# Kernel tuning notes

Hardware: AMD Instinct MI355X
Metric: run time of the kernel (lower is better)

The kernel has to match this reference:

```python
import jax, jax.numpy as jnp
import numpy as np
from functools import partial

K = 3
P = K * K * K          # 27 kernel points
G = 2                  # groups
PAD = 1
STRIDE = 1
DIL = 1
AXIS_SCALE = (0.5, 1.0, 1.0)   # (x, y, z) offset axis scale
CUR_SCALE = 0.5                # warmup scale at global_step=0
EPS = 1e-5


def setup_inputs() -> dict:
    key = jax.random.key(0)
    ks = jax.random.split(key, 8)
    C, OC = 64, 64
    N, D, H, W = 1, 32, 32, 32
    inp = {
        "x": jax.random.normal(ks[0], (N, C, D, H, W), jnp.float32),
        "dw_w": jax.random.normal(ks[1], (C, 1, K, K, K), jnp.float32) * 0.1,
        "gn_w": jnp.ones((C,), jnp.float32),
        "gn_b": jnp.zeros((C,), jnp.float32),
        "inp_w": jax.random.normal(ks[2], (C, C), jnp.float32) * (1.0 / np.sqrt(C)),
        "inp_b": jnp.zeros((C,), jnp.float32),
        # offset/mask weights are zero-init in the module; use small random values
        # so the deformable sampling path is exercised nontrivially.
        "off_w": jax.random.normal(ks[3], (C, G * P * 3), jnp.float32) * 0.01,
        "off_b": jnp.zeros((G * P * 3,), jnp.float32),
        "mask_w": jax.random.normal(ks[4], (C, G * P), jnp.float32) * 0.01,
        "mask_b": jnp.tile(jnp.full((P,), -5.0, jnp.float32).at[P // 2].set(0.0), (G,)),
        "out_w": jax.random.normal(ks[5], (C, OC), jnp.float32) * (1.0 / np.sqrt(C)),
        "out_b": jnp.zeros((OC,), jnp.float32),
    }
    return inp


def _trilinear(vol, loc):
    # vol: [Dp, Hp, Wp, gc]; loc: [..., 3] with (x, y, z) in [-1, 1]
    # grid_sample semantics: align_corners=False, padding_mode='zeros'
    Dp, Hp, Wp, _ = vol.shape
    ix = (loc[..., 0] + 1.0) * 0.5 * Wp - 0.5
    iy = (loc[..., 1] + 1.0) * 0.5 * Hp - 0.5
    iz = (loc[..., 2] + 1.0) * 0.5 * Dp - 0.5
    x0f, y0f, z0f = jnp.floor(ix), jnp.floor(iy), jnp.floor(iz)
    fx, fy, fz = ix - x0f, iy - y0f, iz - z0f
    x0, y0, z0 = x0f.astype(jnp.int32), y0f.astype(jnp.int32), z0f.astype(jnp.int32)
    out = jnp.zeros(loc.shape[:-1] + (vol.shape[-1],), vol.dtype)
    for dz in (0, 1):
        wz = fz if dz else 1.0 - fz
        cz = z0 + dz
        for dy in (0, 1):
            wy = fy if dy else 1.0 - fy
            cy = y0 + dy
            for dx in (0, 1):
                wx = fx if dx else 1.0 - fx
                cx = x0 + dx
                valid = ((cz >= 0) & (cz < Dp) & (cy >= 0) & (cy < Hp)
                         & (cx >= 0) & (cx < Wp))
                v = vol[jnp.clip(cz, 0, Dp - 1),
                        jnp.clip(cy, 0, Hp - 1),
                        jnp.clip(cx, 0, Wp - 1)]  # [..., gc]
                out = out + (wz * wy * wx * valid.astype(vol.dtype))[..., None] * v
    return out


def _forward(x, dw_w, gn_w, gn_b, inp_w, inp_b, off_w, off_b,
             mask_w, mask_b, out_w, out_b):
    N, C, D, H, W = x.shape
    gc = C // G
    # --- dw_conv: depthwise conv3d + GroupNorm(1, C) + GELU ---
    xc = jax.lax.conv_general_dilated(
        x, dw_w, window_strides=(1, 1, 1), padding=[(PAD, PAD)] * 3,
        dimension_numbers=("NCDHW", "OIDHW", "NCDHW"), feature_group_count=C)
    mu = xc.mean(axis=(1, 2, 3, 4), keepdims=True)
    var = ((xc - mu) ** 2).mean(axis=(1, 2, 3, 4), keepdims=True)
    xn = (xc - mu) * jax.lax.rsqrt(var + EPS)
    xn = xn * gn_w[None, :, None, None, None] + gn_b[None, :, None, None, None]
    x1 = jnp.transpose(jax.nn.gelu(xn), (0, 2, 3, 4, 1))       # [N,D,H,W,C]
    # --- offset / mask / input projection ---
    offset = x1 @ off_w + off_b                                  # [N,D,H,W,G*P*3]
    mask = jax.nn.softmax(
        (x1 @ mask_w + mask_b).reshape(N, D, H, W, G, P), axis=-1)
    xp = jnp.transpose(x, (0, 2, 3, 4, 1)) @ inp_w + inp_b       # [N,D,H,W,C]
    # --- core deformable sampling ---
    x_pad = jnp.pad(xp, ((0, 0), (PAD, PAD), (PAD, PAD), (PAD, PAD), (0, 0)))
    Dp, Hp, Wp = D + 2 * PAD, H + 2 * PAD, W + 2 * PAD
    Do = (D + 2 * PAD - DIL * (K - 1) - 1) // STRIDE + 1
    Ho = (H + 2 * PAD - DIL * (K - 1) - 1) // STRIDE + 1
    Wo = (W + 2 * PAD - DIL * (K - 1) - 1) // STRIDE + 1
    # reference grid (x/Wp, y/Hp, z/Dp)
    zc, yc, xc_ = jnp.meshgrid(jnp.arange(Do, dtype=jnp.float32),
                               jnp.arange(Ho, dtype=jnp.float32),
                               jnp.arange(Wo, dtype=jnp.float32), indexing="ij")
    ref = jnp.stack(((xc_ * STRIDE + PAD + 0.5) / Wp,
                     (yc * STRIDE + PAD + 0.5) / Hp,
                     (zc * STRIDE + PAD + 0.5) / Dp), axis=-1)   # [Do,Ho,Wo,3]
    # kernel grid
    lin = jnp.linspace(-(K - 1) // 2, (K - 1) // 2, K, dtype=jnp.float32)
    kz, ky, kx = jnp.meshgrid(lin, lin, lin, indexing="ij")
    kgrid = jnp.stack((kx * DIL / Wp, ky * DIL / Hp, kz * DIL / Dp),
                      axis=-1).reshape(P, 3)
    off = offset.reshape(N, Do, Ho, Wo, G, P, 3)
    off_norm = off / jnp.array([Wp, Hp, Dp], jnp.float32)
    axis = jnp.array(AXIS_SCALE, jnp.float32)
    loc = (ref[None, :, :, :, None, None, :]
           + kgrid[None, None, None, None, None, :, :]
           + off_norm * axis * CUR_SCALE)
    loc = loc * 2.0 - 1.0                                        # [N,Do,Ho,Wo,G,P,3]
    vol = jnp.transpose(x_pad.reshape(N, Dp, Hp, Wp, G, gc),
                        (0, 4, 1, 2, 3, 5))                      # [N,G,Dp,Hp,Wp,gc]
    locs = jnp.transpose(loc, (0, 4, 1, 2, 3, 5, 6))             # [N,G,Do,Ho,Wo,P,3]
    sampled = jax.vmap(jax.vmap(_trilinear))(vol, locs)          # [N,G,Do,Ho,Wo,P,gc]
    out = jnp.einsum("ngdhwpc,ndhwgp->ndhwgc", sampled, mask)
    out = out.reshape(N, Do, Ho, Wo, C)
    return out @ out_w + out_b                                   # [N,Do,Ho,Wo,OC]


def reference(x, dw_w, gn_w, gn_b, inp_w, inp_b, off_w, off_b,
              mask_w, mask_b, out_w, out_b):
    return _forward(x, dw_w, gn_w, gn_b, inp_w, inp_b, off_w, off_b,
                    mask_w, mask_b, out_w, out_b)
```

## Files before the change

### kernel.cpp

```cpp
#include <hip/hip_runtime.h>
#include <hip/hip_fp16.h>
#include <math.h>

#define SP 32768
#define PW 38
#define PW2 (PW*PW)
#define PVOX (PW*PW*PW)
#define OMS 228

typedef short bf16x8 __attribute__((ext_vector_type(8)));
typedef unsigned short u16x4 __attribute__((ext_vector_type(4)));
typedef float f32x4 __attribute__((ext_vector_type(4)));

__device__ __forceinline__ unsigned short f2b(float f) {
    unsigned u = __float_as_uint(f);
    u = (u + 0x7FFFu + ((u >> 16) & 1u)) >> 16;
    return (unsigned short)u;
}
__device__ __forceinline__ float b2f1(unsigned short s) {
    return __uint_as_float(((unsigned)s) << 16);
}
__device__ __forceinline__ __half2 h2(unsigned u) {
    return *reinterpret_cast<__half2*>(&u);
}

__global__ void k_front(const float* __restrict__ x, const float* __restrict__ dw,
                        const float* __restrict__ off_w, const float* __restrict__ mask_w,
                        const float* __restrict__ off_b, const float* __restrict__ mask_b,
                        const float* __restrict__ inp_w, const float* __restrict__ out_w,
                        unsigned short* __restrict__ WcatB, float* __restrict__ bcat,
                        unsigned short* __restrict__ inpB, unsigned short* __restrict__ outB,
                        unsigned short* __restrict__ x_tb,
                        unsigned short* __restrict__ xcb, float* __restrict__ partials) {
    int bb = blockIdx.x, tid = threadIdx.x;
    if (bb < 88) {
        int idx = bb * 256 + tid;
        int j = idx >> 6, k = idx & 63;
        if (j < 224) {
            float v = 0.f;
            if (j < 162) v = off_w[k * 162 + j];
            else if (j < 216) v = mask_w[k * 54 + (j - 162)];
            WcatB[j * 64 + k] = f2b(v);
            if (k == 0) bcat[j] = (j < 162) ? off_b[j] : (j < 216 ? mask_b[j - 162] : 0.f);
        } else if (j < 288) {
            outB[(j - 224) * 64 + k] = f2b(out_w[k * 64 + (j - 224)]);
        } else {
            inpB[(j - 288) * 64 + k] = f2b(inp_w[k * 64 + (j - 288)]);
        }
        return;
    }
    if (bb < 600) {
        __shared__ unsigned short tile[64][66];
        int s0 = (bb - 88) * 64;
        int row = tid >> 6, lane = tid & 63;
        for (int c = row; c < 64; c += 4)
            tile[c][lane] = f2b(x[(size_t)c * SP + s0 + lane]);
        __syncthreads();
        for (int r = row; r < 64; r += 4)
            x_tb[(size_t)(s0 + r) * 64 + lane] = tile[lane][r];
        return;
    }
    int b3 = bb - 600;
    int e = b3 * 256 + tid;
    int c = e >> 15, s = e & 32767;
    int d = s >> 10, h = (s >> 5) & 31, w = s & 31;
    const float* xs = x + (size_t)c * SP;
    const float* wt = dw + c * 27;
    float a = 0.f;
#pragma unroll
    for (int kd = 0; kd < 3; ++kd) {
        int zz = d + kd - 1; if ((unsigned)zz >= 32u) continue;
#pragma unroll
        for (int kh = 0; kh < 3; ++kh) {
            int yy = h + kh - 1; if ((unsigned)yy >= 32u) continue;
#pragma unroll
            for (int kw = 0; kw < 3; ++kw) {
                int xx = w + kw - 1; if ((unsigned)xx >= 32u) continue;
                a += xs[(zz << 10) + (yy << 5) + xx] * wt[kd * 9 + kh * 3 + kw];
            }
        }
    }
    xcb[e] = f2b(a);
    __shared__ float rs[256], rq[256];
    rs[tid] = a; rq[tid] = a * a;
    __syncthreads();
    for (int off = 128; off > 0; off >>= 1) {
        if (tid < off) { rs[tid] += rs[tid + off]; rq[tid] += rq[tid + off]; }
        __syncthreads();
    }
    if (tid == 0) {
        partials[b3 * 2 + 0] = rs[0];
        partials[b3 * 2 + 1] = rq[0];
    }
}

__global__ void k_mid(const unsigned short* __restrict__ xcb, const float* __restrict__ partials,
                      const float* __restrict__ gn_w, const float* __restrict__ gn_b,
                      unsigned short* __restrict__ x1b,
                      const unsigned short* __restrict__ x_tb,
                      const unsigned short* __restrict__ inpB,
                      const float* __restrict__ inp_b,
                      unsigned short* __restrict__ xpad) {
    int bb = blockIdx.x, tid = threadIdx.x;
    if (bb < 512) {
        __shared__ float rs[256], rq[256];
        __shared__ unsigned short tile[64][66];
        float a = 0.f, b = 0.f;
        for (int i = tid; i < 8192; i += 256) { a += partials[2 * i]; b += partials[2 * i + 1]; }
        rs[tid] = a; rq[tid] = b;
        __syncthreads();
        for (int off = 128; off > 0; off >>= 1) {
            if (tid < off) { rs[tid] += rs[tid + off]; rq[tid] += rq[tid + off]; }
            __syncthreads();
        }
        const float Minv = 1.f / 2097152.f;
        float mu = rs[0] * Minv;
        float var = rq[0] * Minv - mu * mu;
        float rsq = rsqrtf(var + 1e-5f);
        int s0 = bb * 64;
        int row = tid >> 6, lane = tid & 63;
        for (int c = row; c < 64; c += 4) {
            float v = (b2f1(xcb[(size_t)c * SP + s0 + lane]) - mu) * rsq * gn_w[c] + gn_b[c];
            float t2 = 1.5957691216057308f * (v + 0.044715f * v * v * v);
            tile[c][lane] = f2b(v / (1.f + __expf(-t2)));
        }
        __syncthreads();
        for (int r = row; r < 64; r += 4)
            x1b[(size_t)(s0 + r) * 64 + lane] = tile[lane][r];
        return;
    }
    if (bb < 1024) {
        int wv = tid >> 6, lane = tid & 63;
        int quad = lane >> 4, col = lane & 15;
        int s0 = (bb - 512) * 64 + wv * 16;
        bf16x8 a0 = *(const bf16x8*)(x_tb + (size_t)(s0 + col) * 64 + quad * 8);
        bf16x8 a1 = *(const bf16x8*)(x_tb + (size_t)(s0 + col) * 64 + 32 + quad * 8);
        int vp[4];
#pragma unroll
        for (int r = 0; r < 4; ++r) {
            int s = s0 + (quad << 2) + r;
            vp[r] = (((s >> 10) + 2) * PW + ((s >> 5) & 31) + 2) * PW + (s & 31) + 2;
        }
#pragma unroll
        for (int nt = 0; nt < 4; ++nt) {
            int n0 = nt * 16;
            bf16x8 b0 = *(const bf16x8*)(inpB + (n0 + col) * 64 + quad * 8);
            bf16x8 b1 = *(const bf16x8*)(inpB + (n0 + col) * 64 + 32 + quad * 8);
            f32x4 c = {0.f, 0.f, 0.f, 0.f};
            c = __builtin_amdgcn_mfma_f32_16x16x32_bf16(a0, b0, c, 0, 0, 0);
            c = __builtin_amdgcn_mfma_f32_16x16x32_bf16(a1, b1, c, 0, 0, 0);
            float bq = inp_b[n0 + col];
#pragma unroll
            for (int r = 0; r < 4; ++r)
                xpad[(size_t)vp[r] * 64 + n0 + col] =
                    __half_as_ushort(__float2half(c[r] + bq));
        }
        return;
    }
    int cblk = bb - 1024;
    int j = tid >> 4, c4 = tid & 15;
    u16x4 z = {0, 0, 0, 0};
#pragma unroll
    for (int k = 0; k < 4; ++k) {
        int v = cblk * 64 + k * 16 + j;
        if (v >= PVOX) break;
        int zz = v / PW2, r = v - zz * PW2, yy = r / PW, xx = r - yy * PW;
        if (zz < 2 || zz > 33 || yy < 2 || yy > 33 || xx < 2 || xx > 33)
            *(u16x4*)(xpad + (size_t)v * 64 + c4 * 4) = z;
    }
}

template<int P0, int NP>
__device__ __forceinline__ void sampleN(const float* __restrict__ orow,
                                        const float* __restrict__ mrow,
                                        const char* __restrict__ volc,
                                        float xb, float yb, float zb,
                                        float* __restrict__ acc) {
#pragma unroll
    for (int i = 0; i < NP; ++i) {
        const int p = P0 + i;
        const int px = p % 3, py = (p / 3) % 3, pz = p / 9;
        float ox = orow[p * 3 + 0], oy = orow[p * 3 + 1], oz = orow[p * 3 + 2];
        float mk = mrow[p];
        float ix = __builtin_fmaf(0.25f, ox, xb + (float)px);
        float iy = __builtin_fmaf(0.5f, oy, yb + (float)py);
        float iz = __builtin_fmaf(0.5f, oz, zb + (float)pz);
        ix = fminf(fmaxf(ix, 0.f), 36.f);
        iy = fminf(fmaxf(iy, 0.f), 36.f);
        iz = fminf(fmaxf(iz, 0.f), 36.f);
        float xf = floorf(ix), yf = floorf(iy), zf = floorf(iz);
        float fx = ix - xf, fy = iy - yf, fz = iz - zf;
        float fi = __builtin_fmaf(zf, (float)PW2, __builtin_fmaf(yf, (float)PW, xf));
        int ib = ((int)fi) << 7;
        const char* base = volc + ib;
        uint4 r000 = *(const uint4*)(base);
        uint4 r001 = *(const uint4*)(base + 128);
        uint4 r010 = *(const uint4*)(base + PW * 128);
        uint4 r011 = *(const uint4*)(base + PW * 128 + 128);
        uint4 r100 = *(const uint4*)(base + PW2 * 128);
        uint4 r101 = *(const uint4*)(base + PW2 * 128 + 128);
        uint4 r110 = *(const uint4*)(base + (PW2 + PW) * 128);
        uint4 r111 = *(const uint4*)(base + (PW2 + PW) * 128 + 128);
        __half2 fx2 = __float2half2_rn(fx);
        __half2 fy2 = __float2half2_rn(fy);
        __half2 fz2 = __float2half2_rn(fz);
        #define TRI(comp, ci)                                                   \
        {                                                                       \
            __half2 t0 = __hfma2(fx2, __hsub2(h2(r001.comp), h2(r000.comp)), h2(r000.comp)); \
            __half2 t1 = __hfma2(fx2, __hsub2(h2(r011.comp), h2(r010.comp)), h2(r010.comp)); \
            __half2 t2 = __hfma2(fx2, __hsub2(h2(r101.comp), h2(r100.comp)), h2(r100.comp)); \
            __half2 t3 = __hfma2(fx2, __hsub2(h2(r111.comp), h2(r110.comp)), h2(r110.comp)); \
            __half2 u0 = __hfma2(fy2, __hsub2(t1, t0), t0);                     \
            __half2 u1 = __hfma2(fy2, __hsub2(t3, t2), t2);                     \
            __half2 rr = __hfma2(fz2, __hsub2(u1, u0), u0);                     \
            float2 ff = __half22float2(rr);                                     \
            acc[2 * ci + 0] = __builtin_fmaf(mk, ff.x, acc[2 * ci + 0]);        \
            acc[2 * ci + 1] = __builtin_fmaf(mk, ff.y, acc[2 * ci + 1]);        \
        }
        TRI(x, 0) TRI(y, 1) TRI(z, 2) TRI(w, 3)
        #undef TRI
    }
}

__global__ void __launch_bounds__(128, 4) k_main(const unsigned short* __restrict__ x1b,
                                                 const unsigned short* __restrict__ xpad,
                                                 const unsigned short* __restrict__ WcatB,
                                                 const float* __restrict__ bcat,
                                                 const unsigned short* __restrict__ outB,
                                                 const float* __restrict__ out_b,
                                                 float* __restrict__ out) {
    __shared__ float om_s[16 * OMS];
    __shared__ unsigned short smb[16 * 72];
    int tid = threadIdx.x, wv = tid >> 6, lane = tid & 63;
    int quad = lane >> 4, col = lane & 15;
    int sb = ((blockIdx.x & 7) << 8) | (blockIdx.x >> 3);
    int s0 = sb * 16;
    {
        bf16x8 a0 = *(const bf16x8*)(x1b + (size_t)(s0 + col) * 64 + quad * 8);
        bf16x8 a1 = *(const bf16x8*)(x1b + (size_t)(s0 + col) * 64 + 32 + quad * 8);
        for (int jt = wv; jt < 14; jt += 2) {
            int n0 = jt * 16;
            bf16x8 b0 = *(const bf16x8*)(WcatB + (n0 + col) * 64 + quad * 8);
            bf16x8 b1 = *(const bf16x8*)(WcatB + (n0 + col) * 64 + 32 + quad * 8);
            f32x4 c = {0.f, 0.f, 0.f, 0.f};
            c = __builtin_amdgcn_mfma_f32_16x16x32_bf16(a0, b0, c, 0, 0, 0);
            c = __builtin_amdgcn_mfma_f32_16x16x32_bf16(a1, b1, c, 0, 0, 0);
            float bb = bcat[n0 + col];
            int n = n0 + col, slot;
            if (n < 162) slot = n + ((n >= 81) ? 3 : 0);
            else { int n2 = n - 162; slot = 168 + n2 + ((n2 >= 27) ? 1 : 0); }
            if (n < 216) {
#pragma unroll
                for (int r = 0; r < 4; ++r)
                    om_s[(quad * 4 + r) * OMS + slot] = c[r] + bb;
            }
        }
    }
    __syncthreads();
    {
        int row = lane >> 2, sub = lane & 3;
        int vloc = wv * 8 + (row >> 1), g = row & 1;
        float* m = &om_s[vloc * OMS + 168 + g * 28];
        float mv[7];
        float mx = -1e30f;
#pragma unroll
        for (int i = 0; i < 7; ++i) {
            int p = sub * 7 + i;
            mv[i] = (p < 27) ? m[p] : -1e30f;
            mx = fmaxf(mx, mv[i]);
        }
        mx = fmaxf(mx, __shfl_xor(mx, 1));
        mx = fmaxf(mx, __shfl_xor(mx, 2));
        float e[7], sm = 0.f;
#pragma unroll
        for (int i = 0; i < 7; ++i) { e[i] = __expf(mv[i] - mx); sm += e[i]; }
        sm += __shfl_xor(sm, 1);
        sm += __shfl_xor(sm, 2);
        float inv = 1.f / sm;
#pragma unroll
        for (int i = 0; i < 7; ++i) {
            int p = sub * 7 + i;
            if (p < 27) m[p] = e[i] * inv;
        }
    }
    {
        int v = wv * 8 + (lane >> 3);
        int oct = lane & 7, gg = oct >> 2;
        int sv = s0 + v;
        float zb = (float)((sv >> 10) + 1);
        float yb = (float)(((sv >> 5) & 31) + 1);
        float xb = (float)((sv & 31) + 1);
        const float* orow = &om_s[v * OMS + gg * 84];
        const float* mrow = &om_s[v * OMS + 168 + gg * 28];
        const char* volc = (const char*)xpad + oct * 16;
        float acc[8] = {0.f, 0.f, 0.f, 0.f, 0.f, 0.f, 0.f, 0.f};
        sampleN<0, 27>(orow, mrow, volc, xb, yb, zb, acc);
        bf16x8 sb8;
#pragma unroll
        for (int k = 0; k < 8; ++k) sb8[k] = (short)f2b(acc[k]);
        *(bf16x8*)(smb + v * 72 + oct * 8) = sb8;
    }
    __syncthreads();
    {
        bf16x8 oa0 = *(const bf16x8*)(smb + col * 72 + quad * 8);
        bf16x8 oa1 = *(const bf16x8*)(smb + col * 72 + 32 + quad * 8);
#pragma unroll
        for (int t = 0; t < 2; ++t) {
            int n0 = (wv + t * 2) * 16;
            bf16x8 b0 = *(const bf16x8*)(outB + (n0 + col) * 64 + quad * 8);
            bf16x8 b1 = *(const bf16x8*)(outB + (n0 + col) * 64 + 32 + quad * 8);
            f32x4 c = {0.f, 0.f, 0.f, 0.f};
            c = __builtin_amdgcn_mfma_f32_16x16x32_bf16(oa0, b0, c, 0, 0, 0);
            c = __builtin_amdgcn_mfma_f32_16x16x32_bf16(oa1, b1, c, 0, 0, 0);
            float bb = out_b[n0 + col];
#pragma unroll
            for (int r = 0; r < 4; ++r)
                out[(size_t)(s0 + quad * 4 + r) * 64 + n0 + col] = c[r] + bb;
        }
    }
}

extern "C" void kernel_launch(void* const* d_in, const int* in_sizes, int n_in,
                              void* d_out, int out_size, void* d_ws, size_t ws_size,
                              hipStream_t stream) {
    const float* x      = (const float*)d_in[0];
    const float* dw_w   = (const float*)d_in[1];
    const float* gn_w   = (const float*)d_in[2];
    const float* gn_b   = (const float*)d_in[3];
    const float* inp_w  = (const float*)d_in[4];
    const float* inp_b  = (const float*)d_in[5];
    const float* off_w  = (const float*)d_in[6];
    const float* off_b  = (const float*)d_in[7];
    const float* mask_w = (const float*)d_in[8];
    const float* mask_b = (const float*)d_in[9];
    const float* out_w  = (const float*)d_in[10];
    const float* out_b  = (const float*)d_in[11];

    char* B = (char*)d_ws;
    float*          partials = (float*)(B + 256);
    unsigned short* xcb      = (unsigned short*)(B + 65792);
    unsigned short* x1b      = (unsigned short*)(B + 8454400);
    unsigned short* x_tb     = (unsigned short*)(B + 12648704);
    unsigned short* xpad     = (unsigned short*)(B + 16843008);
    unsigned short* WcatB    = (unsigned short*)(B + 30890240);
    float*          bcat     = (float*)(B + 30918912);
    unsigned short* inpB     = (unsigned short*)(B + 30919936);
    unsigned short* outB     = (unsigned short*)(B + 30928128);
    float* out = (float*)d_out;

    k_front<<<8792, 256, 0, stream>>>(x, dw_w, off_w, mask_w, off_b, mask_b,
                                      inp_w, out_w, WcatB, bcat, inpB, outB,
                                      x_tb, xcb, partials);
    k_mid<<<512 + 512 + 858, 256, 0, stream>>>(xcb, partials, gn_w, gn_b, x1b,
                                               x_tb, inpB, inp_b, xpad);
    k_main<<<2048, 128, 0, stream>>>(x1b, xpad, WcatB, bcat, outB, out_b, out);
}
```

Baseline: 174.0 us.

## Double threads per block so each sampler lane handles four channels

The main kernel goes from 128 to 256 threads per block. Each deformable-sampling lane now covers 4 fp16 channels with 8-byte corner loads instead of 8 channels with 16-byte loads, which halves per-thread register and arithmetic work and doubles the number of threads in flight to hide gather latency. The softmax, offset GEMM and output GEMM work splits are re-mapped to 4 waves. In exchange, the offset/mask coordinate math is repeated twice as many times and each corner fetch is narrower.

```diff
diff --git a/kernel.cpp b/kernel.cpp
--- a/kernel.cpp
+++ b/kernel.cpp
@@ -170,15 +170,13 @@
     }
 }
 
-template<int P0, int NP>
-__device__ __forceinline__ void sampleN(const float* __restrict__ orow,
-                                        const float* __restrict__ mrow,
-                                        const char* __restrict__ volc,
-                                        float xb, float yb, float zb,
-                                        float* __restrict__ acc) {
-#pragma unroll
-    for (int i = 0; i < NP; ++i) {
-        const int p = P0 + i;
+__device__ __forceinline__ void sample27_4(const float* __restrict__ orow,
+                                           const float* __restrict__ mrow,
+                                           const char* __restrict__ volc,
+                                           float xb, float yb, float zb,
+                                           float* __restrict__ acc) {
+#pragma unroll
+    for (int p = 0; p < 27; ++p) {
         const int px = p % 3, py = (p / 3) % 3, pz = p / 9;
         float ox = orow[p * 3 + 0], oy = orow[p * 3 + 1], oz = orow[p * 3 + 2];
         float mk = mrow[p];
@@ -193,14 +191,14 @@
         float fi = __builtin_fmaf(zf, (float)PW2, __builtin_fmaf(yf, (float)PW, xf));
         int ib = ((int)fi) << 7;
         const char* base = volc + ib;
-        uint4 r000 = *(const uint4*)(base);
-        uint4 r001 = *(const uint4*)(base + 128);
-        uint4 r010 = *(const uint4*)(base + PW * 128);
-        uint4 r011 = *(const uint4*)(base + PW * 128 + 128);
-        uint4 r100 = *(const uint4*)(base + PW2 * 128);
-        uint4 r101 = *(const uint4*)(base + PW2 * 128 + 128);
-        uint4 r110 = *(const uint4*)(base + (PW2 + PW) * 128);
-        uint4 r111 = *(const uint4*)(base + (PW2 + PW) * 128 + 128);
+        uint2 r000 = *(const uint2*)(base);
+        uint2 r001 = *(const uint2*)(base + 128);
+        uint2 r010 = *(const uint2*)(base + PW * 128);
+        uint2 r011 = *(const uint2*)(base + PW * 128 + 128);
+        uint2 r100 = *(const uint2*)(base + PW2 * 128);
+        uint2 r101 = *(const uint2*)(base + PW2 * 128 + 128);
+        uint2 r110 = *(const uint2*)(base + (PW2 + PW) * 128);
+        uint2 r111 = *(const uint2*)(base + (PW2 + PW) * 128 + 128);
         __half2 fx2 = __float2half2_rn(fx);
         __half2 fy2 = __float2half2_rn(fy);
         __half2 fz2 = __float2half2_rn(fz);
@@ -217,12 +215,12 @@
             acc[2 * ci + 0] = __builtin_fmaf(mk, ff.x, acc[2 * ci + 0]);        \
             acc[2 * ci + 1] = __builtin_fmaf(mk, ff.y, acc[2 * ci + 1]);        \
         }
-        TRI(x, 0) TRI(y, 1) TRI(z, 2) TRI(w, 3)
+        TRI(x, 0) TRI(y, 1)
         #undef TRI
     }
 }
 
-__global__ void __launch_bounds__(128, 4) k_main(const unsigned short* __restrict__ x1b,
+__global__ void __launch_bounds__(256, 8) k_main(const unsigned short* __restrict__ x1b,
                                                  const unsigned short* __restrict__ xpad,
                                                  const unsigned short* __restrict__ WcatB,
                                                  const float* __restrict__ bcat,
@@ -238,7 +236,7 @@
     {
         bf16x8 a0 = *(const bf16x8*)(x1b + (size_t)(s0 + col) * 64 + quad * 8);
         bf16x8 a1 = *(const bf16x8*)(x1b + (size_t)(s0 + col) * 64 + 32 + quad * 8);
-        for (int jt = wv; jt < 14; jt += 2) {
+        for (int jt = wv; jt < 14; jt += 4) {
             int n0 = jt * 16;
             bf16x8 b0 = *(const bf16x8*)(WcatB + (n0 + col) * 64 + quad * 8);
             bf16x8 b1 = *(const bf16x8*)(WcatB + (n0 + col) * 64 + 32 + quad * 8);
@@ -258,65 +256,64 @@
     }
     __syncthreads();
     {
-        int row = lane >> 2, sub = lane & 3;
-        int vloc = wv * 8 + (row >> 1), g = row & 1;
+        int row = lane >> 3, sub = lane & 7;
+        int vloc = wv * 4 + (row >> 1), g = row & 1;
         float* m = &om_s[vloc * OMS + 168 + g * 28];
-        float mv[7];
+        float mv[4];
         float mx = -1e30f;
 #pragma unroll
-        for (int i = 0; i < 7; ++i) {
-            int p = sub * 7 + i;
+        for (int i = 0; i < 4; ++i) {
+            int p = sub * 4 + i;
             mv[i] = (p < 27) ? m[p] : -1e30f;
             mx = fmaxf(mx, mv[i]);
         }
         mx = fmaxf(mx, __shfl_xor(mx, 1));
         mx = fmaxf(mx, __shfl_xor(mx, 2));
-        float e[7], sm = 0.f;
-#pragma unroll
-        for (int i = 0; i < 7; ++i) { e[i] = __expf(mv[i] - mx); sm += e[i]; }
+        mx = fmaxf(mx, __shfl_xor(mx, 4));
+        float e[4], sm = 0.f;
+#pragma unroll
+        for (int i = 0; i < 4; ++i) { e[i] = __expf(mv[i] - mx); sm += e[i]; }
         sm += __shfl_xor(sm, 1);
         sm += __shfl_xor(sm, 2);
+        sm += __shfl_xor(sm, 4);
         float inv = 1.f / sm;
 #pragma unroll
-        for (int i = 0; i < 7; ++i) {
-            int p = sub * 7 + i;
+        for (int i = 0; i < 4; ++i) {
+            int p = sub * 4 + i;
             if (p < 27) m[p] = e[i] * inv;
         }
     }
     {
-        int v = wv * 8 + (lane >> 3);
-        int oct = lane & 7, gg = oct >> 2;
+        int v = wv * 4 + (lane >> 4);
+        int oc = lane & 15, gg = oc >> 3;
         int sv = s0 + v;
         float zb = (float)((sv >> 10) + 1);
         float yb = (float)(((sv >> 5) & 31) + 1);
         float xb = (float)((sv & 31) + 1);
         const float* orow = &om_s[v * OMS + gg * 84];
         const float* mrow = &om_s[v * OMS + 168 + gg * 28];
-        const char* volc = (const char*)xpad + oct * 16;
-        float acc[8] = {0.f, 0.f, 0.f, 0.f, 0.f, 0.f, 0.f, 0.f};
-        sampleN<0, 27>(orow, mrow, volc, xb, yb, zb, acc);
-        bf16x8 sb8;
-#pragma unroll
-        for (int k = 0; k < 8; ++k) sb8[k] = (short)f2b(acc[k]);
-        *(bf16x8*)(smb + v * 72 + oct * 8) = sb8;
+        const char* volc = (const char*)xpad + oc * 8;
+        float acc[4] = {0.f, 0.f, 0.f, 0.f};
+        sample27_4(orow, mrow, volc, xb, yb, zb, acc);
+        u16x4 sb4;
+#pragma unroll
+        for (int k = 0; k < 4; ++k) sb4[k] = f2b(acc[k]);
+        *(u16x4*)(smb + v * 72 + oc * 4) = sb4;
     }
     __syncthreads();
     {
         bf16x8 oa0 = *(const bf16x8*)(smb + col * 72 + quad * 8);
         bf16x8 oa1 = *(const bf16x8*)(smb + col * 72 + 32 + quad * 8);
-#pragma unroll
-        for (int t = 0; t < 2; ++t) {
-            int n0 = (wv + t * 2) * 16;
-            bf16x8 b0 = *(const bf16x8*)(outB + (n0 + col) * 64 + quad * 8);
-            bf16x8 b1 = *(const bf16x8*)(outB + (n0 + col) * 64 + 32 + quad * 8);
-            f32x4 c = {0.f, 0.f, 0.f, 0.f};
-            c = __builtin_amdgcn_mfma_f32_16x16x32_bf16(oa0, b0, c, 0, 0, 0);
-            c = __builtin_amdgcn_mfma_f32_16x16x32_bf16(oa1, b1, c, 0, 0, 0);
-            float bb = out_b[n0 + col];
-#pragma unroll
-            for (int r = 0; r < 4; ++r)
-                out[(size_t)(s0 + quad * 4 + r) * 64 + n0 + col] = c[r] + bb;
-        }
+        int n0 = wv * 16;
+        bf16x8 b0 = *(const bf16x8*)(outB + (n0 + col) * 64 + quad * 8);
+        bf16x8 b1 = *(const bf16x8*)(outB + (n0 + col) * 64 + 32 + quad * 8);
+        f32x4 c = {0.f, 0.f, 0.f, 0.f};
+        c = __builtin_amdgcn_mfma_f32_16x16x32_bf16(oa0, b0, c, 0, 0, 0);
+        c = __builtin_amdgcn_mfma_f32_16x16x32_bf16(oa1, b1, c, 0, 0, 0);
+        float bb = out_b[n0 + col];
+#pragma unroll
+        for (int r = 0; r < 4; ++r)
+            out[(size_t)(s0 + quad * 4 + r) * 64 + n0 + col] = c[r] + bb;
     }
 }
 
@@ -353,5 +350,5 @@
                                       x_tb, xcb, partials);
     k_mid<<<512 + 512 + 858, 256, 0, stream>>>(xcb, partials, gn_w, gn_b, x1b,
                                                x_tb, inpB, inp_b, xpad);
-    k_main<<<2048, 128, 0, stream>>>(x1b, xpad, WcatB, bcat, outB, out_b, out);
-}
+    k_main<<<2048, 256, 0, stream>>>(x1b, xpad, WcatB, bcat, outB, out_b, out);
+}
```

After: 211.5 us. 1.22x slower.

## Vectorize depthwise conv, move pad zeroing to front kernel, tile main voxels in 3D

Applied to the files above, without the earlier changes.

The depthwise conv now has each thread compute four adjacent outputs from float4 row loads plus two halo values, so there are fewer threads and partials, and the GN reduction reads fewer partials. Zeroing the xpad border moves from k_mid into k_front. k_main now maps each 16-voxel block to a 4x2x2 spatial brick instead of a 16-voxel row segment. The brick is meant to improve cache locality of the trilinear gathers, at the cost of strided output and x1b accesses.

```diff
diff --git a/kernel.cpp b/kernel.cpp
--- a/kernel.cpp
+++ b/kernel.cpp
@@ -22,6 +22,11 @@
 }
 __device__ __forceinline__ __half2 h2(unsigned u) {
     return *reinterpret_cast<__half2*>(&u);
+}
+__device__ __forceinline__ int vox_of(int sb, int v) {
+    int tw = sb & 7, th = (sb >> 3) & 15, td = sb >> 7;
+    int vw = v & 3, vh = (v >> 2) & 1, vd = v >> 3;
+    return (((td << 1) + vd) << 10) + (((th << 1) + vh) << 5) + (tw << 2) + vw;
 }
 
 __global__ void k_front(const float* __restrict__ x, const float* __restrict__ dw,
@@ -31,7 +36,8 @@
                         unsigned short* __restrict__ WcatB, float* __restrict__ bcat,
                         unsigned short* __restrict__ inpB, unsigned short* __restrict__ outB,
                         unsigned short* __restrict__ x_tb,
-                        unsigned short* __restrict__ xcb, float* __restrict__ partials) {
+                        unsigned short* __restrict__ xcb, float* __restrict__ partials,
+                        unsigned short* __restrict__ xpad) {
     int bb = blockIdx.x, tid = threadIdx.x;
     if (bb < 88) {
         int idx = bb * 256 + tid;
@@ -60,37 +66,58 @@
             x_tb[(size_t)(s0 + r) * 64 + lane] = tile[lane][r];
         return;
     }
-    int b3 = bb - 600;
-    int e = b3 * 256 + tid;
-    int c = e >> 15, s = e & 32767;
-    int d = s >> 10, h = (s >> 5) & 31, w = s & 31;
-    const float* xs = x + (size_t)c * SP;
-    const float* wt = dw + c * 27;
-    float a = 0.f;
-#pragma unroll
-    for (int kd = 0; kd < 3; ++kd) {
-        int zz = d + kd - 1; if ((unsigned)zz >= 32u) continue;
-#pragma unroll
-        for (int kh = 0; kh < 3; ++kh) {
-            int yy = h + kh - 1; if ((unsigned)yy >= 32u) continue;
-#pragma unroll
-            for (int kw = 0; kw < 3; ++kw) {
-                int xx = w + kw - 1; if ((unsigned)xx >= 32u) continue;
-                a += xs[(zz << 10) + (yy << 5) + xx] * wt[kd * 9 + kh * 3 + kw];
+    if (bb < 2648) {
+        int b4 = bb - 600;
+        int e4 = b4 * 256 + tid;
+        int c = e4 >> 13, s4 = (e4 & 8191) << 2;
+        int d = s4 >> 10, h = (s4 >> 5) & 31, w0 = s4 & 31;
+        const float* xs = x + (size_t)c * SP;
+        const float* wt = dw + c * 27;
+        float a0 = 0.f, a1 = 0.f, a2 = 0.f, a3 = 0.f;
+#pragma unroll
+        for (int kd = 0; kd < 3; ++kd) {
+            int zz = d + kd - 1; if ((unsigned)zz >= 32u) continue;
+#pragma unroll
+            for (int kh = 0; kh < 3; ++kh) {
+                int yy = h + kh - 1; if ((unsigned)yy >= 32u) continue;
+                const float* row = xs + (zz << 10) + (yy << 5) + w0;
+                float4 L = *(const float4*)row;
+                float xl = (w0 > 0) ? row[-1] : 0.f;
+                float xr = (w0 < 28) ? row[4] : 0.f;
+                const float* wr = wt + kd * 9 + kh * 3;
+                float wm = wr[0], wc = wr[1], wp = wr[2];
+                a0 = __builtin_fmaf(wm, xl,  __builtin_fmaf(wc, L.x, __builtin_fmaf(wp, L.y, a0)));
+                a1 = __builtin_fmaf(wm, L.x, __builtin_fmaf(wc, L.y, __builtin_fmaf(wp, L.z, a1)));
+                a2 = __builtin_fmaf(wm, L.y, __builtin_fmaf(wc, L.z, __builtin_fmaf(wp, L.w, a2)));
+                a3 = __builtin_fmaf(wm, L.z, __builtin_fmaf(wc, L.w, __builtin_fmaf(wp, xr,  a3)));
             }
         }
-    }
-    xcb[e] = f2b(a);
-    __shared__ float rs[256], rq[256];
-    rs[tid] = a; rq[tid] = a * a;
-    __syncthreads();
-    for (int off = 128; off > 0; off >>= 1) {
-        if (tid < off) { rs[tid] += rs[tid + off]; rq[tid] += rq[tid + off]; }
+        u16x4 o4; o4[0] = f2b(a0); o4[1] = f2b(a1); o4[2] = f2b(a2); o4[3] = f2b(a3);
+        *(u16x4*)(xcb + (size_t)e4 * 4) = o4;
+        __shared__ float rs[256], rq[256];
+        rs[tid] = a0 + a1 + a2 + a3;
+        rq[tid] = a0 * a0 + a1 * a1 + a2 * a2 + a3 * a3;
         __syncthreads();
-    }
-    if (tid == 0) {
-        partials[b3 * 2 + 0] = rs[0];
-        partials[b3 * 2 + 1] = rq[0];
+        for (int off = 128; off > 0; off >>= 1) {
+            if (tid < off) { rs[tid] += rs[tid + off]; rq[tid] += rq[tid + off]; }
+            __syncthreads();
+        }
+        if (tid == 0) {
+            partials[b4 * 2 + 0] = rs[0];
+            partials[b4 * 2 + 1] = rq[0];
+        }
+        return;
+    }
+    int cblk = bb - 2648;
+    int j = tid >> 4, c4 = tid & 15;
+    u16x4 z = {0, 0, 0, 0};
+#pragma unroll
+    for (int k = 0; k < 4; ++k) {
+        int v = cblk * 64 + k * 16 + j;
+        if (v >= PVOX) break;
+        int zz = v / PW2, r = v - zz * PW2, yy = r / PW, xx = r - yy * PW;
+        if (zz < 2 || zz > 33 || yy < 2 || yy > 33 || xx < 2 || xx > 33)
+            *(u16x4*)(xpad + (size_t)v * 64 + c4 * 4) = z;
     }
 }
 
@@ -106,7 +133,7 @@
         __shared__ float rs[256], rq[256];
         __shared__ unsigned short tile[64][66];
         float a = 0.f, b = 0.f;
-        for (int i = tid; i < 8192; i += 256) { a += partials[2 * i]; b += partials[2 * i + 1]; }
+        for (int i = tid; i < 2048; i += 256) { a += partials[2 * i]; b += partials[2 * i + 1]; }
         rs[tid] = a; rq[tid] = b;
         __syncthreads();
         for (int off = 128; off > 0; off >>= 1) {
@@ -129,7 +156,7 @@
             x1b[(size_t)(s0 + r) * 64 + lane] = tile[lane][r];
         return;
     }
-    if (bb < 1024) {
+    {
         int wv = tid >> 6, lane = tid & 63;
         int quad = lane >> 4, col = lane & 15;
         int s0 = (bb - 512) * 64 + wv * 16;
@@ -155,18 +182,6 @@
                 xpad[(size_t)vp[r] * 64 + n0 + col] =
                     __half_as_ushort(__float2half(c[r] + bq));
         }
-        return;
-    }
-    int cblk = bb - 1024;
-    int j = tid >> 4, c4 = tid & 15;
-    u16x4 z = {0, 0, 0, 0};
-#pragma unroll
-    for (int k = 0; k < 4; ++k) {
-        int v = cblk * 64 + k * 16 + j;
-        if (v >= PVOX) break;
-        int zz = v / PW2, r = v - zz * PW2, yy = r / PW, xx = r - yy * PW;
-        if (zz < 2 || zz > 33 || yy < 2 || yy > 33 || xx < 2 || xx > 33)
-            *(u16x4*)(xpad + (size_t)v * 64 + c4 * 4) = z;
     }
 }
 
@@ -234,10 +249,10 @@
     int tid = threadIdx.x, wv = tid >> 6, lane = tid & 63;
     int quad = lane >> 4, col = lane & 15;
     int sb = ((blockIdx.x & 7) << 8) | (blockIdx.x >> 3);
-    int s0 = sb * 16;
-    {
-        bf16x8 a0 = *(const bf16x8*)(x1b + (size_t)(s0 + col) * 64 + quad * 8);
-        bf16x8 a1 = *(const bf16x8*)(x1b + (size_t)(s0 + col) * 64 + 32 + quad * 8);
+    {
+        int sv = vox_of(sb, col);
+        bf16x8 a0 = *(const bf16x8*)(x1b + (size_t)sv * 64 + quad * 8);
+        bf16x8 a1 = *(const bf16x8*)(x1b + (size_t)sv * 64 + 32 + quad * 8);
         for (int jt = wv; jt < 14; jt += 2) {
             int n0 = jt * 16;
             bf16x8 b0 = *(const bf16x8*)(WcatB + (n0 + col) * 64 + quad * 8);
@@ -286,7 +301,7 @@
     {
         int v = wv * 8 + (lane >> 3);
         int oct = lane & 7, gg = oct >> 2;
-        int sv = s0 + v;
+        int sv = vox_of(sb, v);
         float zb = (float)((sv >> 10) + 1);
         float yb = (float)(((sv >> 5) & 31) + 1);
         float xb = (float)((sv & 31) + 1);
@@ -304,6 +319,9 @@
     {
         bf16x8 oa0 = *(const bf16x8*)(smb + col * 72 + quad * 8);
         bf16x8 oa1 = *(const bf16x8*)(smb + col * 72 + 32 + quad * 8);
+        int vr[4];
+#pragma unroll
+        for (int r = 0; r < 4; ++r) vr[r] = vox_of(sb, quad * 4 + r);
 #pragma unroll
         for (int t = 0; t < 2; ++t) {
             int n0 = (wv + t * 2) * 16;
@@ -315,7 +333,7 @@
             float bb = out_b[n0 + col];
 #pragma unroll
             for (int r = 0; r < 4; ++r)
-                out[(size_t)(s0 + quad * 4 + r) * 64 + n0 + col] = c[r] + bb;
+                out[(size_t)vr[r] * 64 + n0 + col] = c[r] + bb;
         }
     }
 }
@@ -348,10 +366,10 @@
     unsigned short* outB     = (unsigned short*)(B + 30928128);
     float* out = (float*)d_out;
 
-    k_front<<<8792, 256, 0, stream>>>(x, dw_w, off_w, mask_w, off_b, mask_b,
-                                      inp_w, out_w, WcatB, bcat, inpB, outB,
-                                      x_tb, xcb, partials);
-    k_mid<<<512 + 512 + 858, 256, 0, stream>>>(xcb, partials, gn_w, gn_b, x1b,
-                                               x_tb, inpB, inp_b, xpad);
+    k_front<<<88 + 512 + 2048 + 858, 256, 0, stream>>>(x, dw_w, off_w, mask_w, off_b, mask_b,
+                                                       inp_w, out_w, WcatB, bcat, inpB, outB,
+                                                       x_tb, xcb, partials, xpad);
+    k_mid<<<512 + 512, 256, 0, stream>>>(xcb, partials, gn_w, gn_b, x1b,
+                                         x_tb, inpB, inp_b, xpad);
     k_main<<<2048, 128, 0, stream>>>(x1b, xpad, WcatB, bcat, outB, out_b, out);
 }
```

Result: faster. 153.5 us (-11.8%).
